# Kernel tuning notes

Hardware: AMD Instinct MI355X
Metric: run time of the kernel (lower is better)

Reference implementation:

```python
import jax, jax.numpy as jnp
import numpy as np

N = 100000      # nodes
DEG = 16        # uniform in-degree
E = N * DEG     # edges
D = 2           # pseudo-coordinate dim
K = 4           # gaussian kernels
IN_F = 128      # input feature dim
OUT_F = 32      # output feature dim


def setup_inputs() -> dict:
    key = jax.random.key(0)
    ks = jax.random.split(key, 6)
    # dst-major CSR: node i owns edges rowptr[i]:rowptr[i+1]
    rowptr = (jnp.arange(N + 1) * DEG).astype(jnp.int32)
    colind = jax.random.randint(ks[0], (E,), 0, N, dtype=jnp.int32)  # src ids
    # CSC mirror (consumed by fused kernel's backward only; not used in fwd math)
    colptr = rowptr
    rowind = colind
    permute = jnp.arange(E, dtype=jnp.int32)  # CSR edge order -> pseudo order
    feat = jax.random.normal(ks[1], (N, IN_F), jnp.float32)
    pseudo = jax.random.normal(ks[2], (E, D), jnp.float32)
    # parameters (per reset_parameters: xavier fc, mu~N(0,0.1), inv_sigma=1, bias=0)
    gain = 1.4142135  # relu gain
    std = gain * (2.0 / (IN_F + K * OUT_F)) ** 0.5
    fc_w = jax.random.normal(ks[3], (K * OUT_F, IN_F), jnp.float32) * std
    mu = jax.random.normal(ks[4], (K, D), jnp.float32) * 0.1
    inv_sigma = jnp.ones((K, D), jnp.float32)
    bias = jnp.zeros((OUT_F,), jnp.float32)
    return {"rowptr": rowptr, "colind": colind, "colptr": colptr,
            "rowind": rowind, "permute": permute, "feat": feat,
            "pseudo": pseudo, "fc_w": fc_w, "mu": mu,
            "inv_sigma": inv_sigma, "bias": bias}


def reference(rowptr, colind, colptr, rowind, permute, feat, pseudo,
              fc_w, mu, inv_sigma, bias):
    n = feat.shape[0]
    e = colind.shape[0]
    k, d = mu.shape
    out_f = bias.shape[0]
    # fc(feat).view(-1, K, OUT)
    node_feat = (feat @ fc_w.T).reshape(n, k, out_f)  # [N,K,F]
    # per-edge gaussian kernel weights from pseudo coords (CSR edge order)
    pe = pseudo[permute]                               # [E,D]
    diff = (pe[:, None, :] - mu[None, :, :]) * inv_sigma[None, :, :]  # [E,K,D]
    w = jnp.exp(-0.5 * jnp.sum(diff * diff, axis=-1))  # [E,K]
    # gather src kernel-features, weight, sum over kernels (.sum(1) commutes)
    msg = jnp.einsum('ek,ekf->ef', w, node_feat[colind])  # [E,F]
    # scatter-sum into dst nodes
    deg = rowptr[1:] - rowptr[:-1]
    dst = jnp.repeat(jnp.arange(n, dtype=jnp.int32), deg, total_repeat_length=e)
    rst = jax.ops.segment_sum(msg, dst, num_segments=n)  # [N,F]
    return rst + bias
```

## Files before the change

### kernel.cpp

```cpp
#include <hip/hip_runtime.h>

#define NN     100000
#define DEG    16
#define IN_F   128
#define OUT_F  32
#define KK     4
#define JDIM   (KK * OUT_F)

typedef __attribute__((ext_vector_type(8))) short short8;
typedef __attribute__((ext_vector_type(4))) short short4v;
typedef __attribute__((ext_vector_type(4))) float floatx4;

static __device__ __forceinline__ unsigned short f2bf(float f) {
  unsigned int u = __builtin_bit_cast(unsigned int, f);
  u += 0x7fffu + ((u >> 16) & 1u);
  return (unsigned short)(u >> 16);
}

__global__ __launch_bounds__(256) void gmm_cvt_w(
    const float* __restrict__ fc_w, unsigned short* __restrict__ wcvt)
{
  const int g = blockIdx.x * 256 + threadIdx.x;
  const int c = g & 15, q = (g >> 4) & 3, t = (g >> 6) & 7, s = g >> 9;
  const float* src = fc_w + (size_t)(t * 16 + c) * IN_F + s * 32 + q * 8;
  const float4 f0 = *(const float4*)src;
  const float4 f1 = *(const float4*)(src + 4);
  short8 v;
  v[0] = (short)f2bf(f0.x); v[1] = (short)f2bf(f0.y);
  v[2] = (short)f2bf(f0.z); v[3] = (short)f2bf(f0.w);
  v[4] = (short)f2bf(f1.x); v[5] = (short)f2bf(f1.y);
  v[6] = (short)f2bf(f1.z); v[7] = (short)f2bf(f1.w);
  *(short8*)(wcvt + (size_t)g * 8) = v;
}

__global__ __launch_bounds__(256) void gmm_fc_mfma(
    const float* __restrict__ feat, const unsigned short* __restrict__ wcvt,
    unsigned short* __restrict__ nf)
{
  const int lane = threadIdx.x & 63;
  const int wv   = threadIdx.x >> 6;
  const int tile = blockIdx.x * 4 + wv;
  if (tile * 16 >= NN) return;
  const int m0 = tile * 16;
  const int c  = lane & 15;
  const int q  = lane >> 4;

  floatx4 acc[8];
#pragma unroll
  for (int t = 0; t < 8; ++t) acc[t] = (floatx4){0.f, 0.f, 0.f, 0.f};

  const float*  frow  = feat + (size_t)(m0 + c) * IN_F + q * 8;
  const short8* wbase = (const short8*)wcvt;

#pragma unroll
  for (int s = 0; s < 4; ++s) {
    const float4 b0 = *(const float4*)(frow + s * 32);
    const float4 b1 = *(const float4*)(frow + s * 32 + 4);
    short8 bv;
    bv[0] = (short)f2bf(b0.x); bv[1] = (short)f2bf(b0.y);
    bv[2] = (short)f2bf(b0.z); bv[3] = (short)f2bf(b0.w);
    bv[4] = (short)f2bf(b1.x); bv[5] = (short)f2bf(b1.y);
    bv[6] = (short)f2bf(b1.z); bv[7] = (short)f2bf(b1.w);
#pragma unroll
    for (int t = 0; t < 8; ++t) {
      const short8 av = wbase[(s * 8 + t) * 64 + lane];
      acc[t] = __builtin_amdgcn_mfma_f32_16x16x32_bf16(av, bv, acc[t], 0, 0, 0);
    }
  }

#pragma unroll
  for (int t = 0; t < 8; ++t) {
    short4v p;
    p[0] = (short)f2bf(acc[t][0]); p[1] = (short)f2bf(acc[t][1]);
    p[2] = (short)f2bf(acc[t][2]); p[3] = (short)f2bf(acc[t][3]);
    *(short4v*)(nf + (size_t)(m0 + c) * JDIM + t * 16 + q * 4) = p;
  }
}

__global__ __launch_bounds__(256) void gmm_edge_gather(
    const int* __restrict__ rowptr, const int* __restrict__ colind,
    const int* __restrict__ permute, const float* __restrict__ pseudo,
    const float* __restrict__ mu, const float* __restrict__ inv_sigma,
    const float* __restrict__ bias, const unsigned short* __restrict__ nf,
    float* __restrict__ out)
{
  __shared__ int   s_src[1024];
  __shared__ float s_w[1024][4];

  const int tid    = threadIdx.x;
  const int node0  = blockIdx.x * 64;
  const int nvalid = (NN - node0 < 64) ? (NN - node0) : 64;

  float mx[KK], my[KK], sx[KK], sy[KK];
#pragma unroll
  for (int k = 0; k < KK; ++k) {
    mx[k] = mu[k * 2 + 0];
    my[k] = mu[k * 2 + 1];
    sx[k] = inv_sigma[k * 2 + 0];
    sy[k] = inv_sigma[k * 2 + 1];
  }

#pragma unroll
  for (int r = 0; r < 4; ++r) {
    const int t  = tid + r * 256;
    const int nl = t >> 4;
    if (nl < nvalid) {
      const int e   = rowptr[node0 + nl] + (t & 15);
      const int pe  = permute[e];
      s_src[t] = colind[e];
      const float px = pseudo[(size_t)pe * 2 + 0];
      const float py = pseudo[(size_t)pe * 2 + 1];
#pragma unroll
      for (int k = 0; k < KK; ++k) {
        const float dx = (px - mx[k]) * sx[k];
        const float dy = (py - my[k]) * sy[k];
        s_w[t][k] = __expf(-0.5f * (dx * dx + dy * dy));
      }
    }
  }
  __syncthreads();

  const int nl = tid >> 2;
  const int f8 = tid & 3;
  if (nl >= nvalid) return;

  float acc[8];
  {
    const float4 b0 = *(const float4*)&bias[f8 * 8];
    const float4 b1 = *(const float4*)&bias[f8 * 8 + 4];
    acc[0] = b0.x; acc[1] = b0.y; acc[2] = b0.z; acc[3] = b0.w;
    acc[4] = b1.x; acc[5] = b1.y; acc[6] = b1.z; acc[7] = b1.w;
  }

  const int tbase = nl * 16;
#pragma unroll
  for (int i = 0; i < DEG; ++i) {
    const int e = (i + nl) & 15;
    const int t = tbase + e;
    const int src = s_src[t];
    const float4 w4 = *(const float4*)&s_w[t][0];
    const float wv[4] = {w4.x, w4.y, w4.z, w4.w};
    const unsigned short* row = nf + (size_t)src * JDIM + f8 * 8;
#pragma unroll
    for (int k = 0; k < KK; ++k) {
      const uint4 v = *(const uint4*)(row + k * 32);
      const float wk = wv[k];
      acc[0] += wk * __uint_as_float(v.x << 16);
      acc[1] += wk * __uint_as_float(v.x & 0xffff0000u);
      acc[2] += wk * __uint_as_float(v.y << 16);
      acc[3] += wk * __uint_as_float(v.y & 0xffff0000u);
      acc[4] += wk * __uint_as_float(v.z << 16);
      acc[5] += wk * __uint_as_float(v.z & 0xffff0000u);
      acc[6] += wk * __uint_as_float(v.w << 16);
      acc[7] += wk * __uint_as_float(v.w & 0xffff0000u);
    }
  }

  float4 o0 = {acc[0], acc[1], acc[2], acc[3]};
  float4 o1 = {acc[4], acc[5], acc[6], acc[7]};
  float* op = out + (size_t)(node0 + nl) * OUT_F + f8 * 8;
  *(float4*)(op)     = o0;
  *(float4*)(op + 4) = o1;
}

extern "C" void kernel_launch(void* const* d_in, const int* in_sizes, int n_in,
                              void* d_out, int out_size, void* d_ws, size_t ws_size,
                              hipStream_t stream) {
  const int*   rowptr    = (const int*)d_in[0];
  const int*   colind    = (const int*)d_in[1];
  const int*   permute   = (const int*)d_in[4];
  const float* feat      = (const float*)d_in[5];
  const float* pseudo    = (const float*)d_in[6];
  const float* fc_w      = (const float*)d_in[7];
  const float* mu        = (const float*)d_in[8];
  const float* inv_sigma = (const float*)d_in[9];
  const float* bias      = (const float*)d_in[10];
  float* out = (float*)d_out;

  unsigned short* nf   = (unsigned short*)d_ws;
  unsigned short* wcvt = (unsigned short*)((char*)d_ws + (26u << 20));

  gmm_cvt_w<<<8, 256, 0, stream>>>(fc_w, wcvt);
  gmm_fc_mfma<<<(NN / 16 + 3) / 4, 256, 0, stream>>>(feat, wcvt, nf);
  gmm_edge_gather<<<(NN + 63) / 64, 256, 0, stream>>>(
      rowptr, colind, permute, pseudo, mu, inv_sigma, bias, nf, out);
}
```

Before: 198.5 us.

## Double-buffer gathered feature rows and compute two row tiles per wave

```diff
diff --git a/kernel.cpp b/kernel.cpp
--- a/kernel.cpp
+++ b/kernel.cpp
@@ -40,40 +40,57 @@
   const int lane = threadIdx.x & 63;
   const int wv   = threadIdx.x >> 6;
   const int tile = blockIdx.x * 4 + wv;
-  if (tile * 16 >= NN) return;
-  const int m0 = tile * 16;
+  if (tile * 32 >= NN) return;
+  const int m0 = tile * 32;
   const int c  = lane & 15;
   const int q  = lane >> 4;
 
-  floatx4 acc[8];
-#pragma unroll
-  for (int t = 0; t < 8; ++t) acc[t] = (floatx4){0.f, 0.f, 0.f, 0.f};
-
-  const float*  frow  = feat + (size_t)(m0 + c) * IN_F + q * 8;
+  floatx4 acc[2][8];
+#pragma unroll
+  for (int g = 0; g < 2; ++g)
+#pragma unroll
+    for (int t = 0; t < 8; ++t) acc[g][t] = (floatx4){0.f, 0.f, 0.f, 0.f};
+
+  const float*  frow0 = feat + (size_t)(m0 + c) * IN_F + q * 8;
+  const float*  frow1 = frow0 + (size_t)16 * IN_F;
   const short8* wbase = (const short8*)wcvt;
 
 #pragma unroll
   for (int s = 0; s < 4; ++s) {
-    const float4 b0 = *(const float4*)(frow + s * 32);
-    const float4 b1 = *(const float4*)(frow + s * 32 + 4);
-    short8 bv;
-    bv[0] = (short)f2bf(b0.x); bv[1] = (short)f2bf(b0.y);
-    bv[2] = (short)f2bf(b0.z); bv[3] = (short)f2bf(b0.w);
-    bv[4] = (short)f2bf(b1.x); bv[5] = (short)f2bf(b1.y);
-    bv[6] = (short)f2bf(b1.z); bv[7] = (short)f2bf(b1.w);
+    short8 bv0, bv1;
+    {
+      const float4 b0 = *(const float4*)(frow0 + s * 32);
+      const float4 b1 = *(const float4*)(frow0 + s * 32 + 4);
+      bv0[0] = (short)f2bf(b0.x); bv0[1] = (short)f2bf(b0.y);
+      bv0[2] = (short)f2bf(b0.z); bv0[3] = (short)f2bf(b0.w);
+      bv0[4] = (short)f2bf(b1.x); bv0[5] = (short)f2bf(b1.y);
+      bv0[6] = (short)f2bf(b1.z); bv0[7] = (short)f2bf(b1.w);
+    }
+    {
+      const float4 b0 = *(const float4*)(frow1 + s * 32);
+      const float4 b1 = *(const float4*)(frow1 + s * 32 + 4);
+      bv1[0] = (short)f2bf(b0.x); bv1[1] = (short)f2bf(b0.y);
+      bv1[2] = (short)f2bf(b0.z); bv1[3] = (short)f2bf(b0.w);
+      bv1[4] = (short)f2bf(b1.x); bv1[5] = (short)f2bf(b1.y);
+      bv1[6] = (short)f2bf(b1.z); bv1[7] = (short)f2bf(b1.w);
+    }
 #pragma unroll
     for (int t = 0; t < 8; ++t) {
       const short8 av = wbase[(s * 8 + t) * 64 + lane];
-      acc[t] = __builtin_amdgcn_mfma_f32_16x16x32_bf16(av, bv, acc[t], 0, 0, 0);
-    }
-  }
-
-#pragma unroll
-  for (int t = 0; t < 8; ++t) {
-    short4v p;
-    p[0] = (short)f2bf(acc[t][0]); p[1] = (short)f2bf(acc[t][1]);
-    p[2] = (short)f2bf(acc[t][2]); p[3] = (short)f2bf(acc[t][3]);
-    *(short4v*)(nf + (size_t)(m0 + c) * JDIM + t * 16 + q * 4) = p;
+      acc[0][t] = __builtin_amdgcn_mfma_f32_16x16x32_bf16(av, bv0, acc[0][t], 0, 0, 0);
+      acc[1][t] = __builtin_amdgcn_mfma_f32_16x16x32_bf16(av, bv1, acc[1][t], 0, 0, 0);
+    }
+  }
+
+#pragma unroll
+  for (int g = 0; g < 2; ++g) {
+#pragma unroll
+    for (int t = 0; t < 8; ++t) {
+      short4v p;
+      p[0] = (short)f2bf(acc[g][t][0]); p[1] = (short)f2bf(acc[g][t][1]);
+      p[2] = (short)f2bf(acc[g][t][2]); p[3] = (short)f2bf(acc[g][t][3]);
+      *(short4v*)(nf + (size_t)(m0 + g * 16 + c) * JDIM + t * 16 + q * 4) = p;
+    }
   }
 }
 
@@ -133,26 +150,40 @@
   }
 
   const int tbase = nl * 16;
+  const char* nfb = (const char*)nf + f8 * 16;
+
+  int off[DEG];
+#pragma unroll
+  for (int i = 0; i < DEG; ++i)
+    off[i] = s_src[tbase + ((i + nl) & 15)] * (JDIM * 2);
+
+  uint4 v[2][KK];
+#pragma unroll
+  for (int k = 0; k < KK; ++k)
+    v[0][k] = *(const uint4*)(nfb + off[0] + k * 64);
+
 #pragma unroll
   for (int i = 0; i < DEG; ++i) {
-    const int e = (i + nl) & 15;
-    const int t = tbase + e;
-    const int src = s_src[t];
-    const float4 w4 = *(const float4*)&s_w[t][0];
+    const int cur = i & 1;
+    if (i + 1 < DEG) {
+#pragma unroll
+      for (int k = 0; k < KK; ++k)
+        v[cur ^ 1][k] = *(const uint4*)(nfb + off[i + 1] + k * 64);
+    }
+    const float4 w4 = *(const float4*)&s_w[tbase + ((i + nl) & 15)][0];
     const float wv[4] = {w4.x, w4.y, w4.z, w4.w};
-    const unsigned short* row = nf + (size_t)src * JDIM + f8 * 8;
 #pragma unroll
     for (int k = 0; k < KK; ++k) {
-      const uint4 v = *(const uint4*)(row + k * 32);
+      const uint4 u = v[cur][k];
       const float wk = wv[k];
-      acc[0] += wk * __uint_as_float(v.x << 16);
-      acc[1] += wk * __uint_as_float(v.x & 0xffff0000u);
-      acc[2] += wk * __uint_as_float(v.y << 16);
-      acc[3] += wk * __uint_as_float(v.y & 0xffff0000u);
-      acc[4] += wk * __uint_as_float(v.z << 16);
-      acc[5] += wk * __uint_as_float(v.z & 0xffff0000u);
-      acc[6] += wk * __uint_as_float(v.w << 16);
-      acc[7] += wk * __uint_as_float(v.w & 0xffff0000u);
+      acc[0] += wk * __uint_as_float(u.x << 16);
+      acc[1] += wk * __uint_as_float(u.x & 0xffff0000u);
+      acc[2] += wk * __uint_as_float(u.y << 16);
+      acc[3] += wk * __uint_as_float(u.y & 0xffff0000u);
+      acc[4] += wk * __uint_as_float(u.z << 16);
+      acc[5] += wk * __uint_as_float(u.z & 0xffff0000u);
+      acc[6] += wk * __uint_as_float(u.w << 16);
+      acc[7] += wk * __uint_as_float(u.w & 0xffff0000u);
     }
   }
 
@@ -181,7 +212,7 @@
   unsigned short* wcvt = (unsigned short*)((char*)d_ws + (26u << 20));
 
   gmm_cvt_w<<<8, 256, 0, stream>>>(fc_w, wcvt);
-  gmm_fc_mfma<<<(NN / 16 + 3) / 4, 256, 0, stream>>>(feat, wcvt, nf);
+  gmm_fc_mfma<<<(NN / 32 + 3) / 4, 256, 0, stream>>>(feat, wcvt, nf);
   gmm_edge_gather<<<(NN + 63) / 64, 256, 0, stream>>>(
       rowptr, colind, permute, pseudo, mu, inv_sigma, bias, nf, out);
 }
```

Measured after the change: 202.1 us. About the same (+1.8%).

## Stage bf16 weight fragments in LDS and compute two 16-row tiles per wave

Applied to the files above, without the earlier changes.

```diff
diff --git a/kernel.cpp b/kernel.cpp
--- a/kernel.cpp
+++ b/kernel.cpp
@@ -37,43 +37,77 @@
     const float* __restrict__ feat, const unsigned short* __restrict__ wcvt,
     unsigned short* __restrict__ nf)
 {
-  const int lane = threadIdx.x & 63;
-  const int wv   = threadIdx.x >> 6;
+  __shared__ uint4 s_wfrag[2048];
+
+  const int tid  = threadIdx.x;
+  const int lane = tid & 63;
+  const int wv   = tid >> 6;
+
+  const uint4* wsrc = (const uint4*)wcvt;
+#pragma unroll
+  for (int r = 0; r < 8; ++r)
+    s_wfrag[tid + r * 256] = wsrc[tid + r * 256];
+  __syncthreads();
+
   const int tile = blockIdx.x * 4 + wv;
-  if (tile * 16 >= NN) return;
-  const int m0 = tile * 16;
+  if (tile * 32 >= NN) return;
+  const int m0 = tile * 32;
   const int c  = lane & 15;
   const int q  = lane >> 4;
 
-  floatx4 acc[8];
-#pragma unroll
-  for (int t = 0; t < 8; ++t) acc[t] = (floatx4){0.f, 0.f, 0.f, 0.f};
-
-  const float*  frow  = feat + (size_t)(m0 + c) * IN_F + q * 8;
-  const short8* wbase = (const short8*)wcvt;
-
+  const float* frow0 = feat + (size_t)(m0 + c) * IN_F + q * 8;
+  const float* frow1 = frow0 + (size_t)16 * IN_F;
+  float4 fr[2][4][2];
 #pragma unroll
   for (int s = 0; s < 4; ++s) {
-    const float4 b0 = *(const float4*)(frow + s * 32);
-    const float4 b1 = *(const float4*)(frow + s * 32 + 4);
-    short8 bv;
-    bv[0] = (short)f2bf(b0.x); bv[1] = (short)f2bf(b0.y);
-    bv[2] = (short)f2bf(b0.z); bv[3] = (short)f2bf(b0.w);
-    bv[4] = (short)f2bf(b1.x); bv[5] = (short)f2bf(b1.y);
-    bv[6] = (short)f2bf(b1.z); bv[7] = (short)f2bf(b1.w);
+    fr[0][s][0] = *(const float4*)(frow0 + s * 32);
+    fr[0][s][1] = *(const float4*)(frow0 + s * 32 + 4);
+    fr[1][s][0] = *(const float4*)(frow1 + s * 32);
+    fr[1][s][1] = *(const float4*)(frow1 + s * 32 + 4);
+  }
+
+  short8 bv[2][4];
+#pragma unroll
+  for (int g = 0; g < 2; ++g) {
+#pragma unroll
+    for (int s = 0; s < 4; ++s) {
+      const float4 b0 = fr[g][s][0];
+      const float4 b1 = fr[g][s][1];
+      short8 v;
+      v[0] = (short)f2bf(b0.x); v[1] = (short)f2bf(b0.y);
+      v[2] = (short)f2bf(b0.z); v[3] = (short)f2bf(b0.w);
+      v[4] = (short)f2bf(b1.x); v[5] = (short)f2bf(b1.y);
+      v[6] = (short)f2bf(b1.z); v[7] = (short)f2bf(b1.w);
+      bv[g][s] = v;
+    }
+  }
+
+  floatx4 acc[2][8];
+#pragma unroll
+  for (int g = 0; g < 2; ++g)
+#pragma unroll
+    for (int t = 0; t < 8; ++t) acc[g][t] = (floatx4){0.f, 0.f, 0.f, 0.f};
+
+  const short8* wlds = (const short8*)s_wfrag;
+#pragma unroll
+  for (int s = 0; s < 4; ++s) {
 #pragma unroll
     for (int t = 0; t < 8; ++t) {
-      const short8 av = wbase[(s * 8 + t) * 64 + lane];
-      acc[t] = __builtin_amdgcn_mfma_f32_16x16x32_bf16(av, bv, acc[t], 0, 0, 0);
-    }
-  }
-
-#pragma unroll
-  for (int t = 0; t < 8; ++t) {
-    short4v p;
-    p[0] = (short)f2bf(acc[t][0]); p[1] = (short)f2bf(acc[t][1]);
-    p[2] = (short)f2bf(acc[t][2]); p[3] = (short)f2bf(acc[t][3]);
-    *(short4v*)(nf + (size_t)(m0 + c) * JDIM + t * 16 + q * 4) = p;
+      const short8 av = wlds[(s * 8 + t) * 64 + lane];
+      acc[0][t] = __builtin_amdgcn_mfma_f32_16x16x32_bf16(av, bv[0][s], acc[0][t], 0, 0, 0);
+      acc[1][t] = __builtin_amdgcn_mfma_f32_16x16x32_bf16(av, bv[1][s], acc[1][t], 0, 0, 0);
+    }
+  }
+
+#pragma unroll
+  for (int g = 0; g < 2; ++g) {
+#pragma unroll
+    for (int t = 0; t < 8; ++t) {
+      short4v p;
+      p[0] = (short)f2bf(acc[g][t][0]); p[1] = (short)f2bf(acc[g][t][1]);
+      p[2] = (short)f2bf(acc[g][t][2]); p[3] = (short)f2bf(acc[g][t][3]);
+      *(short4v*)(nf + (size_t)(m0 + g * 16 + c) * JDIM + t * 16 + q * 4) = p;
+    }
   }
 }
 
@@ -181,7 +215,7 @@
   unsigned short* wcvt = (unsigned short*)((char*)d_ws + (26u << 20));
 
   gmm_cvt_w<<<8, 256, 0, stream>>>(fc_w, wcvt);
-  gmm_fc_mfma<<<(NN / 16 + 3) / 4, 256, 0, stream>>>(feat, wcvt, nf);
+  gmm_fc_mfma<<<(NN / 32 + 3) / 4, 256, 0, stream>>>(feat, wcvt, nf);
   gmm_edge_gather<<<(NN + 63) / 64, 256, 0, stream>>>(
       rowptr, colind, permute, pseudo, mu, inv_sigma, bias, nf, out);
 }
```

New measurement: 194.4 us. -2.1%, faster.
